# Kernel tuning notes

Measured on AMD Instinct MI355X. Metric: run time of the kernel, lower is better.

Reference implementation:

```python
import jax, jax.numpy as jnp
import numpy as np

M, H, D, P = 16, 32, 128, 8192
N = H * D


def setup_inputs() -> dict:
    key = jax.random.key(0)
    ks = jax.random.split(key, 8)
    w_scale = 0.3 / np.sqrt(N)  # keep q,k ~ N(0, 0.3^2) so exp(c) stays finite
    X = jax.random.normal(ks[0], (M, N), jnp.float32)
    Wq = jax.random.normal(ks[1], (N, N), jnp.float32) * w_scale
    Wk = jax.random.normal(ks[2], (N, N), jnp.float32) * w_scale
    Wv = jax.random.normal(ks[3], (N, N), jnp.float32) * w_scale
    cache_K = jax.random.normal(ks[4], (H, P, D), jnp.float32) * 0.3
    cache_V = jax.random.normal(ks[5], (H, P, D), jnp.float32) * 0.3
    tau = jnp.float32(2.0)
    noise = jax.random.normal(ks[6], (H, M, P + M), jnp.float32) * 0.1
    return {"X": X, "Wq": Wq, "Wk": Wk, "Wv": Wv,
            "cache_K": cache_K, "cache_V": cache_V, "tau": tau, "noise": noise}


def reference(X, Wq, Wk, Wv, cache_K, cache_V, tau, noise):
    h, p, d = cache_K.shape
    m, n = X.shape
    # RMS-style prenorm: X / sqrt(mean(X^2, dim=1))
    x_norm = X * jax.lax.rsqrt(jnp.sum(X * X, axis=1, keepdims=True) / n)
    # nn.Linear: y = x @ W^T; reshape to [H, M, D]
    q = (x_norm @ Wq.T).reshape(m, h, d).transpose(1, 0, 2)
    k = (x_norm @ Wk.T).reshape(m, h, d).transpose(1, 0, 2)
    v = (x_norm @ Wv.T).reshape(m, h, d).transpose(1, 0, 2)
    k_cache = jnp.concatenate([cache_K, k], axis=1)  # [H, P+M, D]
    v_cache = jnp.concatenate([cache_V, v], axis=1)
    c = jnp.einsum('hmd,hpd->hmp', q, k_cache)  # [H, M, P+M]
    c_exp = jnp.exp(c)
    c_exp_perturb = jnp.exp((c + noise) / tau)
    c_div = c_exp / jnp.sum(c_exp, axis=2, keepdims=True)
    c_div_perturb = c_exp_perturb / jnp.sum(c_exp_perturb, axis=2, keepdims=True)
    c_out = jnp.sum(c_div_perturb, axis=1)  # [H, P+M]
    o = jnp.einsum('hmp,hpd->hmd', c_div, v_cache)  # [H, M, D]
    o2 = o.transpose(1, 0, 2).reshape(m, n)
    return o2, c_out
```

## Files before the change

kernel.cpp:

```cpp
#include <hip/hip_runtime.h>

#define M_ 16
#define H_ 32
#define D_ 128
#define P_ 8192
#define N_ 4096
#define PM_ 8208

#define WS_Q    0
#define WS_K    65536
#define WS_V    131072
#define WS_S1   196608
#define WS_S2   197120
#define WS_IS2  197632
#define WS_XQ   198144
#define WS_E2   263680
#define WS_PP   263680
#define WS_PO   4466176
#define WS_SP1  6563328
#define WS_SP2  6628864

typedef __attribute__((address_space(1))) const void gvoid_t;
typedef __attribute__((address_space(3))) void lvoid_t;

__global__ __launch_bounds__(256) void rmsnorm_kernel(const float* __restrict__ X,
                                                      float* __restrict__ ws) {
  int m = blockIdx.x, t = threadIdx.x;
  __shared__ float red[256];
  const float4* X4 = (const float4*)(X + (size_t)m * N_);
  float s = 0.f;
  #pragma unroll
  for (int q = 0; q < 4; q++) {
    float4 v = X4[t + q * 256];
    s += v.x * v.x + v.y * v.y + v.z * v.z + v.w * v.w;
  }
  red[t] = s;
  __syncthreads();
  for (int off = 128; off > 0; off >>= 1) {
    if (t < off) red[t] += red[t + off];
    __syncthreads();
  }
  float scale = rsqrtf(red[0] * (1.0f / N_));
  float4* xq = (float4*)(ws + WS_XQ);
  #pragma unroll
  for (int q = 0; q < 4; q++) {
    int nq = t + q * 256;
    float4 v = X4[nq];
    v.x *= scale; v.y *= scale; v.z *= scale; v.w *= scale;
    xq[nq * 16 + m] = v;
  }
}

__global__ __launch_bounds__(256, 4) void proj_kernel(const float* __restrict__ Wq,
                                                      const float* __restrict__ Wk,
                                                      const float* __restrict__ Wv,
                                                      const float* __restrict__ xr,
                                                      float* __restrict__ ws) {
  __shared__ float tile[4 * 2048];
  int widx = threadIdx.x >> 6, lane = threadIdx.x & 63;
  int kc = blockIdx.x / 48;
  int jt = (blockIdx.x % 48) * 4 + widx;
  int jj0 = jt * 64;
  int sel = jj0 >> 12;
  int j0 = jj0 & 4095;
  const float* Wm = (sel == 0) ? Wq : ((sel == 1) ? Wk : Wv);
  int n0 = kc * 256;

  float* tl = tile + widx * 2048;
  int g8 = lane >> 3, c8 = lane & 7;
  int cq = c8 ^ g8;

  const float* gsrc[8];
  #pragma unroll
  for (int i = 0; i < 8; i++)
    gsrc[i] = Wm + (size_t)(j0 + i * 8 + g8) * N_ + n0 + cq * 4;

  const float4* tl4 = (const float4*)tl;
  int rbase = lane * 8;
  int swz = lane & 7;

  const float4* xr4 = (const float4*)xr;
  float acc[16];
  #pragma unroll
  for (int m = 0; m < 16; m++) acc[m] = 0.f;

  for (int ti = 0; ti < 8; ti++) {
    #pragma unroll
    for (int i = 0; i < 8; i++)
      __builtin_amdgcn_global_load_lds((gvoid_t*)(gsrc[i] + ti * 32),
                                       (lvoid_t*)(tl + i * 256), 16, 0, 0);
    asm volatile("s_waitcnt vmcnt(0)" ::: "memory");
    __builtin_amdgcn_sched_barrier(0);

    int nqb = (n0 >> 2) + ti * 8;
    #pragma unroll
    for (int k = 0; k < 8; k++) {
      float4 w4 = tl4[rbase + (k ^ swz)];
      int qbase = (nqb + k) * 16;
      #pragma unroll
      for (int m = 0; m < 16; m++) {
        float4 xm = xr4[qbase + m];
        acc[m] += xm.x * w4.x + xm.y * w4.y + xm.z * w4.z + xm.w * w4.w;
      }
    }
  }

  float* pp = ws + WS_PP + (size_t)kc * 16 * 12288 + jj0 + lane;
  #pragma unroll
  for (int m = 0; m < 16; m++) pp[(size_t)m * 12288] = acc[m];
}

__global__ __launch_bounds__(256) void proj_reduce_kernel(float* __restrict__ ws) {
  int tid = blockIdx.x * 256 + threadIdx.x;
  int m = tid / 12288;
  int j = tid - m * 12288;
  float acc = 0.f;
  #pragma unroll
  for (int kc = 0; kc < 16; kc++)
    acc += ws[WS_PP + ((size_t)(kc * 16 + m)) * 12288 + j];
  int sel = j >> 12, jj = j & 4095;
  int h = jj >> 7, d = jj & 127;
  ws[WS_Q + sel * 65536 + (h * 16 + m) * 128 + d] = acc;
}

__global__ __launch_bounds__(256) void noise_t_kernel(const float* __restrict__ noise,
                                                      float* __restrict__ ws) {
  __shared__ float tile[16 * 68];
  int blk = blockIdx.x;
  int h = blk / 129, ct = blk % 129;
  int c0 = ct * 64;
  int t = threadIdx.x;
  int rw = t >> 6, cc = t & 63;
  #pragma unroll
  for (int i = 0; i < 4; i++) {
    int m = i * 4 + rw;
    int c = c0 + cc;
    if (c < PM_) tile[m * 68 + cc] = noise[((size_t)h * 16 + m) * PM_ + c];
  }
  __syncthreads();
  float* outh = ws + WS_E2 + (size_t)h * PM_ * 16;
  #pragma unroll
  for (int i = 0; i < 4; i++) {
    int flat = i * 256 + t;
    int c = flat >> 4, m = flat & 15;
    if (c0 + c < PM_) outh[(size_t)(c0 + c) * 16 + m] = tile[m * 68 + c];
  }
}

__global__ __launch_bounds__(256) void attn_kernel(const float* __restrict__ cacheK,
                                                   const float* __restrict__ cacheV,
                                                   const float* __restrict__ taup,
                                                   float* __restrict__ ws) {
  __shared__ float red[4 * 2048];
  int h = blockIdx.x >> 5, b = blockIdx.x & 31;
  int widx = threadIdx.x >> 6, lane = threadIdx.x & 63;
  int m8 = lane & 7, sl = lane >> 3;
  int rsel = lane >> 4;
  bool tb = (lane >> 3) & 1;
  bool rb0 = rsel & 1, rb1 = (rsel >> 1) & 1;
  float inv_tau = 1.0f / taup[0];

  float qv[2][16];
  #pragma unroll
  for (int t = 0; t < 2; t++) {
    const float4* qp = (const float4*)(ws + WS_Q + ((size_t)(h * 16) + m8 + 8 * t) * 128 + sl * 16);
    #pragma unroll
    for (int jq = 0; jq < 4; jq++) {
      float4 v = qp[jq];
      qv[t][jq * 4] = v.x; qv[t][jq * 4 + 1] = v.y;
      qv[t][jq * 4 + 2] = v.z; qv[t][jq * 4 + 3] = v.w;
    }
  }
  float oacc[2][16];
  #pragma unroll
  for (int t = 0; t < 2; t++)
    #pragma unroll
    for (int j = 0; j < 16; j++) oacc[t][j] = 0.f;
  float s1 = 0.f, s2 = 0.f;

  float* e2g = ws + WS_E2 + (size_t)h * PM_ * 16 + lane;
  const float* kc_base = cacheK + (size_t)h * P_ * D_;
  const float* vc_base = cacheV + (size_t)h * P_ * D_;
  const float* kn_base = ws + WS_K + (size_t)h * 16 * 128;
  const float* vn_base = ws + WS_V + (size_t)h * 16 * 128;

  auto kvp = [&](int p0, const float*& kb, const float*& vb) {
    if (p0 < P_) { kb = kc_base + (size_t)p0 * D_; vb = vc_base + (size_t)p0 * D_; }
    else { kb = kn_base + (size_t)(p0 - P_) * D_; vb = vn_base + (size_t)(p0 - P_) * D_; }
  };
  auto dotrows = [&](const float* kb, float (&pr)[4][2]) {
    #pragma unroll
    for (int r = 0; r < 4; r++) {
      float4 kq[4];
      const float4* krp = (const float4*)(kb + r * D_ + sl * 16);
      kq[0] = krp[0]; kq[1] = krp[1]; kq[2] = krp[2]; kq[3] = krp[3];
      const float* kk = (const float*)kq;
      float t0 = 0.f, t1 = 0.f;
      #pragma unroll
      for (int j = 0; j < 16; j++) { t0 += kk[j] * qv[0][j]; t1 += kk[j] * qv[1][j]; }
      pr[r][0] = t0; pr[r][1] = t1;
    }
  };
  auto finish = [&](float (&pr)[4][2], float nz, int p0, const float* vb) {
    float cc[4][2];
    #pragma unroll
    for (int r = 0; r < 4; r++)
      #pragma unroll
      for (int t = 0; t < 2; t++) {
        float v = pr[r][t];
        v += __shfl_xor(v, 8, 64);
        v += __shfl_xor(v, 16, 64);
        v += __shfl_xor(v, 32, 64);
        cc[r][t] = v;
      }
    float a0 = tb ? cc[0][1] : cc[0][0];
    float a1 = tb ? cc[1][1] : cc[1][0];
    float a2 = tb ? cc[2][1] : cc[2][0];
    float a3 = tb ? cc[3][1] : cc[3][0];
    float b0 = rb0 ? a1 : a0;
    float b1 = rb0 ? a3 : a2;
    float myc = rb1 ? b1 : b0;

    float e2 = __expf((myc + nz) * inv_tau);
    e2g[(size_t)p0 * 16] = e2;
    s2 += e2;

    float e1[4][2];
    #pragma unroll
    for (int r = 0; r < 4; r++) {
      e1[r][0] = __expf(cc[r][0]);
      e1[r][1] = __expf(cc[r][1]);
    }
    float f0 = tb ? e1[0][1] : e1[0][0];
    float f1 = tb ? e1[1][1] : e1[1][0];
    float f2 = tb ? e1[2][1] : e1[2][0];
    float f3 = tb ? e1[3][1] : e1[3][0];
    float g0s = rb0 ? f1 : f0;
    float g1s = rb0 ? f3 : f2;
    s1 += rb1 ? g1s : g0s;

    #pragma unroll
    for (int r = 0; r < 4; r++) {
      float4 vq[4];
      const float4* vrp = (const float4*)(vb + r * D_ + sl * 16);
      vq[0] = vrp[0]; vq[1] = vrp[1]; vq[2] = vrp[2]; vq[3] = vrp[3];
      const float* vv = (const float*)vq;
      float ea = e1[r][0], eb = e1[r][1];
      #pragma unroll
      for (int j = 0; j < 16; j++) {
        oacc[0][j] += ea * vv[j];
        oacc[1][j] += eb * vv[j];
      }
    }
  };

  int g0 = b * 64;
  int gN = (b == 31) ? 68 : 64;
  int gl = widx;
  for (; gl + 4 < gN; gl += 8) {
    int pA = (g0 + gl) * 4, pB = (g0 + gl + 4) * 4;
    const float *kbA, *vbA, *kbB, *vbB;
    kvp(pA, kbA, vbA);
    kvp(pB, kbB, vbB);
    float nzA = e2g[(size_t)pA * 16];
    float nzB = e2g[(size_t)pB * 16];
    float prA[4][2], prB[4][2];
    dotrows(kbA, prA);
    dotrows(kbB, prB);
    finish(prA, nzA, pA, vbA);
    finish(prB, nzB, pB, vbB);
  }
  if (gl < gN) {
    int pA = (g0 + gl) * 4;
    const float *kbA, *vbA;
    kvp(pA, kbA, vbA);
    float nzA = e2g[(size_t)pA * 16];
    float prA[4][2];
    dotrows(kbA, prA);
    finish(prA, nzA, pA, vbA);
  }

  s1 += __shfl_xor(s1, 16, 64); s1 += __shfl_xor(s1, 32, 64);
  s2 += __shfl_xor(s2, 16, 64); s2 += __shfl_xor(s2, 32, 64);
  if (lane < 16) {
    size_t sp = ((size_t)h * 128 + b * 4 + widx) * 16 + lane;
    ws[WS_SP1 + sp] = s1;
    ws[WS_SP2 + sp] = s2;
  }

  float* rw = red + widx * 2048 + lane * 32;
  #pragma unroll
  for (int t = 0; t < 2; t++)
    #pragma unroll
    for (int j = 0; j < 16; j++) {
      int i = t * 16 + j;
      rw[(i + lane) & 31] = oacc[t][j];
    }
  __syncthreads();

  float* po = ws + WS_PO + (size_t)(h * 32 + b) * 2048;
  for (int e = threadIdx.x; e < 2048; e += 256) {
    int ln = e >> 5, i = e & 31;
    int phys = (ln << 5) + ((i + ln) & 31);
    float v = red[phys] + red[phys + 2048] + red[phys + 4096] + red[phys + 6144];
    int mo = (ln & 7) + 8 * (i >> 4);
    int d = (ln >> 3) * 16 + (i & 15);
    po[mo * 128 + d] = v;
  }
}

__global__ __launch_bounds__(256) void sums_kernel(float* __restrict__ ws) {
  int tid = blockIdx.x * 256 + threadIdx.x;
  if (tid >= 512) return;
  int h = tid >> 4, m = tid & 15;
  float a = 0.f, c2 = 0.f;
  for (int i = 0; i < 128; i++) {
    a  += ws[WS_SP1 + ((size_t)h * 128 + i) * 16 + m];
    c2 += ws[WS_SP2 + ((size_t)h * 128 + i) * 16 + m];
  }
  ws[WS_S1 + tid] = a;
  ws[WS_S2 + tid] = c2;
  ws[WS_IS2 + tid] = 1.0f / c2;
}

__global__ __launch_bounds__(256) void epilogue_kernel(const float* __restrict__ ws,
                                                       float* __restrict__ out) {
  int tid = blockIdx.x * 256 + threadIdx.x;
  int mm = tid >> 12, j = tid & 4095;
  int h = j >> 7, d = j & 127;
  float acc = 0.f;
  #pragma unroll
  for (int b = 0; b < 32; b++)
    acc += ws[WS_PO + (size_t)(h * 32 + b) * 2048 + mm * 128 + d];
  out[tid] = acc / ws[WS_S1 + h * 16 + mm];
}

__global__ __launch_bounds__(256) void cout_kernel(const float* __restrict__ ws,
                                                   float* __restrict__ out) {
  int tid = blockIdx.x * 256 + threadIdx.x;
  if (tid >= H_ * PM_) return;
  int h = tid / PM_, p = tid - h * PM_;
  const float4* e2p = (const float4*)(ws + WS_E2 + ((size_t)h * PM_ + p) * 16);
  const float* is2 = ws + WS_IS2 + h * 16;
  float acc = 0.f;
  #pragma unroll
  for (int q = 0; q < 4; q++) {
    float4 v = e2p[q];
    acc += v.x * is2[q * 4] + v.y * is2[q * 4 + 1] + v.z * is2[q * 4 + 2] + v.w * is2[q * 4 + 3];
  }
  out[65536 + tid] = acc;
}

extern "C" void kernel_launch(void* const* d_in, const int* in_sizes, int n_in,
                              void* d_out, int out_size, void* d_ws, size_t ws_size,
                              hipStream_t stream) {
  const float* X     = (const float*)d_in[0];
  const float* Wq    = (const float*)d_in[1];
  const float* Wk    = (const float*)d_in[2];
  const float* Wv    = (const float*)d_in[3];
  const float* cK    = (const float*)d_in[4];
  const float* cV    = (const float*)d_in[5];
  const float* tau   = (const float*)d_in[6];
  const float* noise = (const float*)d_in[7];
  float* out = (float*)d_out;
  float* ws  = (float*)d_ws;

  rmsnorm_kernel<<<16, 256, 0, stream>>>(X, ws);
  proj_kernel<<<768, 256, 0, stream>>>(Wq, Wk, Wv, ws + WS_XQ, ws);
  proj_reduce_kernel<<<768, 256, 0, stream>>>(ws);
  noise_t_kernel<<<32 * 129, 256, 0, stream>>>(noise, ws);
  attn_kernel<<<1024, 256, 0, stream>>>(cK, cV, tau, ws);
  sums_kernel<<<2, 256, 0, stream>>>(ws);
  epilogue_kernel<<<256, 256, 0, stream>>>(ws, out);
  cout_kernel<<<1026, 256, 0, stream>>>(ws, out);
}
```

Before: 259.6 us.

## Double split-K in projection and use 8-wave attention blocks

The projection GEMV now splits the reduction dimension into 32 chunks of 128 instead of 16 chunks of 256, which doubles the grid to 1536 blocks and halves the work per block. proj_reduce and the workspace partial-sum layout are adjusted to match. The attention kernel moves from 4 to 8 waves per block, replaces the manual two-groups-per-iteration unroll with a simple strided loop, and reduces the per-wave output in two LDS passes (one per 8-row half) so the shared buffer stays the same size. The aim is more waves in flight to hide memory latency on both streaming stages. The cost is double the partial-sum traffic for the projection, less instruction-level parallelism per wave in attention, and an extra barrier phase in its reduction.

```diff
diff --git a/kernel.cpp b/kernel.cpp
--- a/kernel.cpp
+++ b/kernel.cpp
@@ -18,7 +18,7 @@
 #define WS_PP   263680
 #define WS_PO   4466176
 #define WS_SP1  6563328
-#define WS_SP2  6628864
+#define WS_SP2  6694400
 
 typedef __attribute__((address_space(1))) const void gvoid_t;
 typedef __attribute__((address_space(3))) void lvoid_t;
@@ -64,7 +64,7 @@
   int sel = jj0 >> 12;
   int j0 = jj0 & 4095;
   const float* Wm = (sel == 0) ? Wq : ((sel == 1) ? Wk : Wv);
-  int n0 = kc * 256;
+  int n0 = kc * 128;
 
   float* tl = tile + widx * 2048;
   int g8 = lane >> 3, c8 = lane & 7;
@@ -84,7 +84,7 @@
   #pragma unroll
   for (int m = 0; m < 16; m++) acc[m] = 0.f;
 
-  for (int ti = 0; ti < 8; ti++) {
+  for (int ti = 0; ti < 4; ti++) {
     #pragma unroll
     for (int i = 0; i < 8; i++)
       __builtin_amdgcn_global_load_lds((gvoid_t*)(gsrc[i] + ti * 32),
@@ -116,7 +116,7 @@
   int j = tid - m * 12288;
   float acc = 0.f;
   #pragma unroll
-  for (int kc = 0; kc < 16; kc++)
+  for (int kc = 0; kc < 32; kc++)
     acc += ws[WS_PP + ((size_t)(kc * 16 + m)) * 12288 + j];
   int sel = j >> 12, jj = j & 4095;
   int h = jj >> 7, d = jj & 127;
@@ -147,11 +147,11 @@
   }
 }
 
-__global__ __launch_bounds__(256) void attn_kernel(const float* __restrict__ cacheK,
+__global__ __launch_bounds__(512) void attn_kernel(const float* __restrict__ cacheK,
                                                    const float* __restrict__ cacheV,
                                                    const float* __restrict__ taup,
                                                    float* __restrict__ ws) {
-  __shared__ float red[4 * 2048];
+  __shared__ float red[8 * 1024];
   int h = blockIdx.x >> 5, b = blockIdx.x & 31;
   int widx = threadIdx.x >> 6, lane = threadIdx.x & 63;
   int m8 = lane & 7, sl = lane >> 3;
@@ -184,11 +184,17 @@
   const float* kn_base = ws + WS_K + (size_t)h * 16 * 128;
   const float* vn_base = ws + WS_V + (size_t)h * 16 * 128;
 
-  auto kvp = [&](int p0, const float*& kb, const float*& vb) {
+  int g0 = b * 64;
+  int gN = (b == 31) ? 68 : 64;
+  for (int gl = widx; gl < gN; gl += 8) {
+    int p0 = (g0 + gl) * 4;
+    const float *kb, *vb;
     if (p0 < P_) { kb = kc_base + (size_t)p0 * D_; vb = vc_base + (size_t)p0 * D_; }
     else { kb = kn_base + (size_t)(p0 - P_) * D_; vb = vn_base + (size_t)(p0 - P_) * D_; }
-  };
-  auto dotrows = [&](const float* kb, float (&pr)[4][2]) {
+
+    float nz = e2g[(size_t)p0 * 16];
+
+    float pr[4][2];
     #pragma unroll
     for (int r = 0; r < 4; r++) {
       float4 kq[4];
@@ -200,8 +206,6 @@
       for (int j = 0; j < 16; j++) { t0 += kk[j] * qv[0][j]; t1 += kk[j] * qv[1][j]; }
       pr[r][0] = t0; pr[r][1] = t1;
     }
-  };
-  auto finish = [&](float (&pr)[4][2], float nz, int p0, const float* vb) {
     float cc[4][2];
     #pragma unroll
     for (int r = 0; r < 4; r++)
@@ -213,6 +217,7 @@
         v += __shfl_xor(v, 32, 64);
         cc[r][t] = v;
       }
+
     float a0 = tb ? cc[0][1] : cc[0][0];
     float a1 = tb ? cc[1][1] : cc[1][0];
     float a2 = tb ? cc[2][1] : cc[2][0];
@@ -252,60 +257,34 @@
         oacc[1][j] += eb * vv[j];
       }
     }
-  };
-
-  int g0 = b * 64;
-  int gN = (b == 31) ? 68 : 64;
-  int gl = widx;
-  for (; gl + 4 < gN; gl += 8) {
-    int pA = (g0 + gl) * 4, pB = (g0 + gl + 4) * 4;
-    const float *kbA, *vbA, *kbB, *vbB;
-    kvp(pA, kbA, vbA);
-    kvp(pB, kbB, vbB);
-    float nzA = e2g[(size_t)pA * 16];
-    float nzB = e2g[(size_t)pB * 16];
-    float prA[4][2], prB[4][2];
-    dotrows(kbA, prA);
-    dotrows(kbB, prB);
-    finish(prA, nzA, pA, vbA);
-    finish(prB, nzB, pB, vbB);
-  }
-  if (gl < gN) {
-    int pA = (g0 + gl) * 4;
-    const float *kbA, *vbA;
-    kvp(pA, kbA, vbA);
-    float nzA = e2g[(size_t)pA * 16];
-    float prA[4][2];
-    dotrows(kbA, prA);
-    finish(prA, nzA, pA, vbA);
   }
 
   s1 += __shfl_xor(s1, 16, 64); s1 += __shfl_xor(s1, 32, 64);
   s2 += __shfl_xor(s2, 16, 64); s2 += __shfl_xor(s2, 32, 64);
   if (lane < 16) {
-    size_t sp = ((size_t)h * 128 + b * 4 + widx) * 16 + lane;
+    size_t sp = (((size_t)h * 32 + b) * 8 + widx) * 16 + lane;
     ws[WS_SP1 + sp] = s1;
     ws[WS_SP2 + sp] = s2;
   }
 
-  float* rw = red + widx * 2048 + lane * 32;
-  #pragma unroll
-  for (int t = 0; t < 2; t++)
-    #pragma unroll
-    for (int j = 0; j < 16; j++) {
-      int i = t * 16 + j;
-      rw[(i + lane) & 31] = oacc[t][j];
-    }
-  __syncthreads();
-
   float* po = ws + WS_PO + (size_t)(h * 32 + b) * 2048;
-  for (int e = threadIdx.x; e < 2048; e += 256) {
-    int ln = e >> 5, i = e & 31;
-    int phys = (ln << 5) + ((i + ln) & 31);
-    float v = red[phys] + red[phys + 2048] + red[phys + 4096] + red[phys + 6144];
-    int mo = (ln & 7) + 8 * (i >> 4);
-    int d = (ln >> 3) * 16 + (i & 15);
-    po[mo * 128 + d] = v;
+  #pragma unroll
+  for (int t = 0; t < 2; t++) {
+    if (t) __syncthreads();
+    float* rw = red + widx * 1024 + lane * 16;
+    #pragma unroll
+    for (int j = 0; j < 16; j++) rw[(j + lane) & 15] = oacc[t][j];
+    __syncthreads();
+    for (int e = threadIdx.x; e < 1024; e += 512) {
+      int ln = e >> 4, j = e & 15;
+      int phys = (ln << 4) + ((j + ln) & 15);
+      float v = 0.f;
+      #pragma unroll
+      for (int w = 0; w < 8; w++) v += red[w * 1024 + phys];
+      int mo = (ln & 7) + 8 * t;
+      int d = (ln >> 3) * 16 + j;
+      po[mo * 128 + d] = v;
+    }
   }
 }
 
@@ -314,9 +293,9 @@
   if (tid >= 512) return;
   int h = tid >> 4, m = tid & 15;
   float a = 0.f, c2 = 0.f;
-  for (int i = 0; i < 128; i++) {
-    a  += ws[WS_SP1 + ((size_t)h * 128 + i) * 16 + m];
-    c2 += ws[WS_SP2 + ((size_t)h * 128 + i) * 16 + m];
+  for (int i = 0; i < 256; i++) {
+    a  += ws[WS_SP1 + ((size_t)h * 256 + i) * 16 + m];
+    c2 += ws[WS_SP2 + ((size_t)h * 256 + i) * 16 + m];
   }
   ws[WS_S1 + tid] = a;
   ws[WS_S2 + tid] = c2;
@@ -366,10 +345,10 @@
   float* ws  = (float*)d_ws;
 
   rmsnorm_kernel<<<16, 256, 0, stream>>>(X, ws);
-  proj_kernel<<<768, 256, 0, stream>>>(Wq, Wk, Wv, ws + WS_XQ, ws);
+  proj_kernel<<<1536, 256, 0, stream>>>(Wq, Wk, Wv, ws + WS_XQ, ws);
   proj_reduce_kernel<<<768, 256, 0, stream>>>(ws);
   noise_t_kernel<<<32 * 129, 256, 0, stream>>>(noise, ws);
-  attn_kernel<<<1024, 256, 0, stream>>>(cK, cV, tau, ws);
+  attn_kernel<<<1024, 512, 0, stream>>>(cK, cV, tau, ws);
   sums_kernel<<<2, 256, 0, stream>>>(ws);
   epilogue_kernel<<<256, 256, 0, stream>>>(ws, out);
   cout_kernel<<<1026, 256, 0, stream>>>(ws, out);
```

After: 302.6 us. +16.6%, slower.
